# Kernel optimization log

Measured on AMD Instinct MI355X. Metric: run time of the kernel, lower is better.

The kernel has to match this reference:

```python
import jax, jax.numpy as jnp
import numpy as np

B, N, D = 8, 512, 768
HS = 64          # gp_head_size
NT = 12          # len(tag_vocab)
NEG = 1e12


def setup_inputs() -> dict:
    key = jax.random.key(0)
    ks = jax.random.split(key, 14)
    s = 0.02  # init scale for weights
    return {
        "chars": jax.random.normal(ks[0], (B, N, D), dtype=jnp.float32),
        "mask": jax.random.randint(ks[1], (B, N), 0, 2).astype(jnp.int32),
        "w1_ent": jax.random.normal(ks[2], (2 * HS, D), dtype=jnp.float32) * s,
        "b1_ent": jax.random.normal(ks[3], (2 * HS,), dtype=jnp.float32) * s,
        "w2_ent": jax.random.normal(ks[4], (2 * 2, 2 * HS), dtype=jnp.float32) * s,
        "b2_ent": jax.random.normal(ks[5], (2 * 2,), dtype=jnp.float32) * s,
        "w1_head": jax.random.normal(ks[6], (2 * HS, D), dtype=jnp.float32) * s,
        "b1_head": jax.random.normal(ks[7], (2 * HS,), dtype=jnp.float32) * s,
        "w2_head": jax.random.normal(ks[8], (2 * NT, 2 * HS), dtype=jnp.float32) * s,
        "b2_head": jax.random.normal(ks[9], (2 * NT,), dtype=jnp.float32) * s,
        "w1_tail": jax.random.normal(ks[10], (2 * HS, D), dtype=jnp.float32) * s,
        "b1_tail": jax.random.normal(ks[11], (2 * HS,), dtype=jnp.float32) * s,
        "w2_tail": jax.random.normal(ks[12], (2 * NT, 2 * HS), dtype=jnp.float32) * s,
        "b2_tail": jax.random.normal(ks[13], (2 * NT,), dtype=jnp.float32) * s,
    }


def _egp(x, w1, b1, w2, b2, mask, head_size, rope, tril):
    # x: [B,N,D] -> h: [B,N,2*head_size]
    h = jnp.einsum('bnd,ed->bne', x, w1) + b1
    qw, kw = h[..., 0::2], h[..., 1::2]          # [B,N,head_size] each
    if rope:
        n = x.shape[1]
        pos = jnp.arange(n, dtype=x.dtype)
        inv = jnp.power(10000.0, -2.0 * jnp.arange(head_size // 2, dtype=x.dtype) / head_size)
        ang = pos[:, None] * inv[None, :]         # [N, head_size/2]
        cos = jnp.repeat(jnp.cos(ang), 2, axis=-1)[None]  # [1,N,head_size]
        sin = jnp.repeat(jnp.sin(ang), 2, axis=-1)[None]
        def rot(t):
            t2 = jnp.stack([-t[..., 1::2], t[..., 0::2]], axis=-1).reshape(t.shape)
            return t * cos + t2 * sin
        qw, kw = rot(qw), rot(kw)
    logits = jnp.einsum('bmd,bnd->bmn', qw, kw) / (head_size ** 0.5)  # [B,M,N]
    bias = (jnp.einsum('bne,he->bnh', h, w2) + b2).transpose(0, 2, 1) / 2.0  # [B,2H,N]
    # [B,H,M,N]
    logits = logits[:, None] + bias[:, 0::2, None, :] + bias[:, 1::2, :, None]
    m = mask.astype(logits.dtype)
    pad = 1.0 - m[:, None, None, :] * m[:, None, :, None]
    logits = logits - pad * NEG
    if tril:
        tri = jnp.tril(jnp.ones((logits.shape[-2], logits.shape[-1]), logits.dtype), k=-1)
        logits = logits - tri * NEG
    return logits


def reference(chars, mask, w1_ent, b1_ent, w2_ent, b2_ent,
              w1_head, b1_head, w2_head, b2_head,
              w1_tail, b1_tail, w2_tail, b2_tail):
    entity = _egp(chars, w1_ent, b1_ent, w2_ent, b2_ent, mask, HS, True, True)
    head = _egp(chars, w1_head, b1_head, w2_head, b2_head, mask, HS, False, False)
    tail = _egp(chars, w1_tail, b1_tail, w2_tail, b2_tail, mask, HS, False, False)
    return (entity, head, tail)
```

## Files before the change

kernel.cpp:

```cpp
#include <hip/hip_runtime.h>
#include <cstddef>

namespace {
constexpr int B_ = 8;
constexpr int N_ = 512;
constexpr int D_ = 768;
constexpr int HS_ = 64;
constexpr int M_ = B_ * N_;
constexpr int E_ = 2 * HS_;
constexpr float NEGV = 1000000000000.0f;
constexpr float LOG2_10000 = 13.287712379549449f;
}

typedef short mfrag_t __attribute__((ext_vector_type(8)));
typedef short mhalf_t __attribute__((ext_vector_type(4)));
typedef float macc_t  __attribute__((ext_vector_type(4)));
typedef float vf4_t   __attribute__((ext_vector_type(4)));

__device__ __forceinline__ unsigned short bft(float x) {
    union { float f; unsigned u; } c; c.f = x;
    return (unsigned short)(c.u >> 16);
}
__device__ __forceinline__ unsigned short bfrne(float x) {
    union { float f; unsigned u; } c; c.f = x;
    const unsigned r = c.u + 0x7FFFu + ((c.u >> 16) & 1u);
    return (unsigned short)(r >> 16);
}

__global__ __launch_bounds__(256) void prep_kernel(
    const float* __restrict__ chars,
    const float* __restrict__ w1e, const float* __restrict__ b1e,
    const float* __restrict__ w2e, const float* __restrict__ b2e,
    const float* __restrict__ w1h, const float* __restrict__ b1h,
    const float* __restrict__ w2h, const float* __restrict__ b2h,
    const float* __restrict__ w1t, const float* __restrict__ b1t,
    const float* __restrict__ w2t, const float* __restrict__ b2t,
    unsigned short* __restrict__ qbf, unsigned short* __restrict__ kbf,
    float* __restrict__ bias_e, float* __restrict__ bias_h, float* __restrict__ bias_t)
{
    const int fam = blockIdx.y;
    const float* w1 = (fam == 0) ? w1e : (fam == 1) ? w1h : w1t;
    const float* b1 = (fam == 0) ? b1e : (fam == 1) ? b1h : b1t;
    const float* w2 = (fam == 0) ? w2e : (fam == 1) ? w2h : w2t;
    const float* b2 = (fam == 0) ? b2e : (fam == 1) ? b2h : b2t;
    float* bout = (fam == 0) ? bias_e : (fam == 1) ? bias_h : bias_t;
    const int H2 = (fam == 0) ? 4 : 24;
    unsigned short* qout = qbf + (size_t)fam * M_ * HS_;
    unsigned short* kout = kbf + (size_t)fam * M_ * HS_;
    const int m0 = blockIdx.x * 32;

    __shared__ unsigned short A_lds[32][40];
    __shared__ unsigned short B_lds[128][40];
    __shared__ float hs[32][132];

    const int t    = threadIdx.x;
    const int w    = t >> 6;
    const int lane = t & 63;
    const int ml   = lane & 15;
    const int quad = lane >> 4;
    const int wr16 = (w & 1) * 16;
    const int wc64 = (w >> 1) * 64;

    const int ar = t >> 3;
    const int ak = (t & 7) * 4;
    const int bc = t >> 1;
    const int bk = (t & 1) * 16;

    const float* aptr = chars + (size_t)(m0 + ar) * D_ + ak;
    const float* bptr = w1 + (size_t)bc * D_ + bk;

    macc_t acc[4];
    #pragma unroll
    for (int f = 0; f < 4; ++f) acc[f] = (macc_t)0.0f;

    float4 av0 = *(const float4*)(aptr);
    float4 bv0 = *(const float4*)(bptr);
    float4 bv1 = *(const float4*)(bptr + 4);
    float4 bv2 = *(const float4*)(bptr + 8);
    float4 bv3 = *(const float4*)(bptr + 12);

    for (int s = 0; s < 24; ++s) {
        {
            mhalf_t pa;
            pa[0] = (short)bft(av0.x); pa[1] = (short)bft(av0.y);
            pa[2] = (short)bft(av0.z); pa[3] = (short)bft(av0.w);
            *(mhalf_t*)&A_lds[ar][ak] = pa;
            mfrag_t pb0, pb1;
            pb0[0] = (short)bft(bv0.x); pb0[1] = (short)bft(bv0.y);
            pb0[2] = (short)bft(bv0.z); pb0[3] = (short)bft(bv0.w);
            pb0[4] = (short)bft(bv1.x); pb0[5] = (short)bft(bv1.y);
            pb0[6] = (short)bft(bv1.z); pb0[7] = (short)bft(bv1.w);
            pb1[0] = (short)bft(bv2.x); pb1[1] = (short)bft(bv2.y);
            pb1[2] = (short)bft(bv2.z); pb1[3] = (short)bft(bv2.w);
            pb1[4] = (short)bft(bv3.x); pb1[5] = (short)bft(bv3.y);
            pb1[6] = (short)bft(bv3.z); pb1[7] = (short)bft(bv3.w);
            *(mfrag_t*)&B_lds[bc][bk]     = pb0;
            *(mfrag_t*)&B_lds[bc][bk + 8] = pb1;
        }
        __syncthreads();
        if (s < 23) {
            aptr += 32; bptr += 32;
            av0 = *(const float4*)(aptr);
            bv0 = *(const float4*)(bptr);
            bv1 = *(const float4*)(bptr + 4);
            bv2 = *(const float4*)(bptr + 8);
            bv3 = *(const float4*)(bptr + 12);
        }
        const mfrag_t afrag = *(const mfrag_t*)&A_lds[wr16 + ml][quad * 8];
        #pragma unroll
        for (int f = 0; f < 4; ++f) {
            const mfrag_t bfrag = *(const mfrag_t*)&B_lds[wc64 + f * 16 + ml][quad * 8];
            acc[f] = __builtin_amdgcn_mfma_f32_16x16x32_bf16(afrag, bfrag, acc[f], 0, 0, 0);
        }
        __syncthreads();
    }

    #pragma unroll
    for (int f = 0; f < 4; ++f) {
        const int col = wc64 + f * 16 + ml;
        const float bb1 = b1[col];
        #pragma unroll
        for (int r = 0; r < 4; ++r)
            hs[wr16 + quad * 4 + r][col] = acc[f][r] + bb1;
    }
    __syncthreads();

    {
        const int row = t >> 3;
        const int kg  = t & 7;
        const float pos = (float)((m0 & 511) + row);
        unsigned short qv[8], kv[8];
        #pragma unroll
        for (int p = 0; p < 4; ++p) {
            const int i = kg * 4 + p;
            const float q0 = hs[row][4 * i + 0];
            const float k0 = hs[row][4 * i + 1];
            const float q1 = hs[row][4 * i + 2];
            const float k1 = hs[row][4 * i + 3];
            if (fam == 0) {
                const float inv = exp2f(-(float)i * (LOG2_10000 / 32.0f));
                float sn, cs;
                sincosf(pos * inv, &sn, &cs);
                qv[2 * p + 0] = bfrne(q0 * cs - q1 * sn);
                qv[2 * p + 1] = bfrne(q1 * cs + q0 * sn);
                kv[2 * p + 0] = bfrne(k0 * cs - k1 * sn);
                kv[2 * p + 1] = bfrne(k1 * cs + k0 * sn);
            } else {
                qv[2 * p + 0] = bfrne(q0);
                qv[2 * p + 1] = bfrne(q1);
                kv[2 * p + 0] = bfrne(k0);
                kv[2 * p + 1] = bfrne(k1);
            }
        }
        unsigned short* qp = qout + (size_t)(m0 + row) * HS_ + kg * 8;
        unsigned short* kp = kout + (size_t)(m0 + row) * HS_ + kg * 8;
        *(mfrag_t*)qp = *(const mfrag_t*)&qv[0];
        *(mfrag_t*)kp = *(const mfrag_t*)&kv[0];
    }

    {
        const int row = t & 31;
        const int h2b = t >> 5;
        const int bb  = m0 >> 9;
        const int nb  = (m0 & 511) + row;
        float accv[3] = {0, 0, 0};
        for (int e0 = 0; e0 < E_; e0 += 16) {
            float4 hv0 = *(const float4*)&hs[row][e0];
            float4 hv1 = *(const float4*)&hs[row][e0 + 4];
            float4 hv2 = *(const float4*)&hs[row][e0 + 8];
            float4 hv3 = *(const float4*)&hs[row][e0 + 12];
            int p = 0;
            for (int h2 = h2b; h2 < H2; h2 += 8, ++p) {
                const float* wr = w2 + (size_t)h2 * E_ + e0;
                const float4 w0 = *(const float4*)(wr);
                const float4 w1v = *(const float4*)(wr + 4);
                const float4 w2v = *(const float4*)(wr + 8);
                const float4 w3v = *(const float4*)(wr + 12);
                accv[p] += hv0.x * w0.x + hv0.y * w0.y + hv0.z * w0.z + hv0.w * w0.w
                         + hv1.x * w1v.x + hv1.y * w1v.y + hv1.z * w1v.z + hv1.w * w1v.w
                         + hv2.x * w2v.x + hv2.y * w2v.y + hv2.z * w2v.z + hv2.w * w2v.w
                         + hv3.x * w3v.x + hv3.y * w3v.y + hv3.z * w3v.z + hv3.w * w3v.w;
            }
        }
        int p = 0;
        for (int h2 = h2b; h2 < H2; h2 += 8, ++p)
            bout[((size_t)bb * H2 + h2) * N_ + nb] = (accv[p] + b2[h2]) * 0.5f;
    }
}

template <int H, bool TRIL>
__device__ __forceinline__ void egp_tile(
    const unsigned short* __restrict__ qf, const unsigned short* __restrict__ kf,
    const float* __restrict__ biasfam, const int* __restrict__ mask,
    float* __restrict__ out, int b, int m0, int n0, float (*Cs)[68], int t)
{
    const int w    = t >> 6;
    const int lane = t & 63;
    const int ml   = lane & 15;
    const int quad = lane >> 4;

    macc_t acc[4];
    #pragma unroll
    for (int f = 0; f < 4; ++f) acc[f] = (macc_t)0.0f;

    const unsigned short* qrow = qf + (size_t)(b * N_ + m0 + w * 16 + ml) * HS_ + quad * 8;
    const unsigned short* krow = kf + (size_t)(b * N_ + n0 + ml) * HS_ + quad * 8;

    #pragma unroll
    for (int s = 0; s < 2; ++s) {
        const mfrag_t af = *(const mfrag_t*)(qrow + s * 32);
        #pragma unroll
        for (int f = 0; f < 4; ++f) {
            const mfrag_t bf = *(const mfrag_t*)(krow + (size_t)f * 16 * HS_ + s * 32);
            acc[f] = __builtin_amdgcn_mfma_f32_16x16x32_bf16(af, bf, acc[f], 0, 0, 0);
        }
    }

    #pragma unroll
    for (int f = 0; f < 4; ++f)
        #pragma unroll
        for (int r = 0; r < 4; ++r)
            Cs[w * 16 + quad * 4 + r][f * 16 + ml] = acc[f][r] * 0.125f;
    __syncthreads();

    const int rq = t >> 4;
    const int cq = t & 15;

    float4 av[4];
    #pragma unroll
    for (int j = 0; j < 4; ++j) av[j] = *(const float4*)&Cs[4 * rq + j][4 * cq];

    int mrow[4], mm[4];
    #pragma unroll
    for (int j = 0; j < 4; ++j) {
        mrow[j] = m0 + 4 * rq + j;
        mm[j]   = mask[b * N_ + mrow[j]];
    }
    const int ncol = n0 + 4 * cq;
    const int4 mnv = *(const int4*)(mask + b * N_ + ncol);
    const int mn[4] = { mnv.x, mnv.y, mnv.z, mnv.w };

    #pragma unroll
    for (int hh = 0; hh < H; ++hh) {
        const float4 be = *(const float4*)(biasfam + ((size_t)b * 2 * H + 2 * hh) * N_ + ncol);
        float bo[4];
        #pragma unroll
        for (int j = 0; j < 4; ++j)
            bo[j] = biasfam[((size_t)b * 2 * H + 2 * hh + 1) * N_ + mrow[j]];

        #pragma unroll
        for (int j = 0; j < 4; ++j) {
            const float* aj = (const float*)&av[j];
            float o[4] = { aj[0] + be.x + bo[j], aj[1] + be.y + bo[j],
                           aj[2] + be.z + bo[j], aj[3] + be.w + bo[j] };
            #pragma unroll
            for (int q = 0; q < 4; ++q) {
                if (!(mm[j] & mn[q])) o[q] -= NEGV;
                if (TRIL && (ncol + q) < mrow[j]) o[q] -= NEGV;
            }
            vf4_t ov;
            ov.x = o[0]; ov.y = o[1]; ov.z = o[2]; ov.w = o[3];
            __builtin_nontemporal_store(
                ov, (vf4_t*)(out + ((size_t)(b * H + hh) * N_ + mrow[j]) * N_ + ncol));
        }
    }
}

__global__ __launch_bounds__(256) void egp_all_kernel(
    const unsigned short* __restrict__ qbf, const unsigned short* __restrict__ kbf,
    const float* __restrict__ bias_e, const float* __restrict__ bias_h,
    const float* __restrict__ bias_t,
    const int* __restrict__ mask, float* __restrict__ out)
{
    __shared__ float Cs[64][68];

    const int t   = threadIdx.x;
    const int m0  = blockIdx.x * 64;
    const int n0  = blockIdx.y * 64;
    const int fam = blockIdx.z >> 3;
    const int b   = blockIdx.z & 7;

    const size_t ent_sz  = (size_t)B_ * 2 * N_ * N_;
    const size_t head_sz = (size_t)B_ * 12 * N_ * N_;
    const size_t fsl = (size_t)M_ * HS_;

    if (fam == 0) {
        egp_tile<2, true>(qbf, kbf, bias_e, mask, out, b, m0, n0, Cs, t);
    } else if (fam == 1) {
        egp_tile<12, false>(qbf + fsl, kbf + fsl, bias_h, mask,
                            out + ent_sz, b, m0, n0, Cs, t);
    } else {
        egp_tile<12, false>(qbf + 2 * fsl, kbf + 2 * fsl, bias_t, mask,
                            out + ent_sz + head_sz, b, m0, n0, Cs, t);
    }
}

extern "C" void kernel_launch(void* const* d_in, const int* in_sizes, int n_in,
                              void* d_out, int out_size, void* d_ws, size_t ws_size,
                              hipStream_t stream)
{
    const float* chars = (const float*)d_in[0];
    const int*   mask  = (const int*)d_in[1];
    const float* w1e = (const float*)d_in[2];
    const float* b1e = (const float*)d_in[3];
    const float* w2e = (const float*)d_in[4];
    const float* b2e = (const float*)d_in[5];
    const float* w1h = (const float*)d_in[6];
    const float* b1h = (const float*)d_in[7];
    const float* w2h = (const float*)d_in[8];
    const float* b2h = (const float*)d_in[9];
    const float* w1t = (const float*)d_in[10];
    const float* b1t = (const float*)d_in[11];
    const float* w2t = (const float*)d_in[12];
    const float* b2t = (const float*)d_in[13];

    float* out = (float*)d_out;

    unsigned short* qbf = (unsigned short*)d_ws;
    unsigned short* kbf = qbf + (size_t)3 * M_ * HS_;
    float* bias_e = (float*)(kbf + (size_t)3 * M_ * HS_);
    float* bias_h = bias_e + (size_t)B_ * 4 * N_;
    float* bias_t = bias_h + (size_t)B_ * 24 * N_;

    prep_kernel<<<dim3(128, 3), 256, 0, stream>>>(
        chars, w1e, b1e, w2e, b2e, w1h, b1h, w2h, b2h, w1t, b1t, w2t, b2t,
        qbf, kbf, bias_e, bias_h, bias_t);

    egp_all_kernel<<<dim3(8, 8, 24), 256, 0, stream>>>(
        qbf, kbf, bias_e, bias_h, bias_t, mask, out);
}
```

Baseline: 283.1 us.

## Split prep kernel output columns in half to double block count

The prep kernel now splits the 128-wide projection output into two 64-column halves handled by separate blocks, doubling the grid from 384 to 768 blocks. Each half writes a partial bias sum to its own buffer, and the main kernel adds the two partial bias buffers when reading them. This is meant to improve occupancy and parallelism of the small projection GEMM on the many-CU GPU. In exchange, the chars tile is loaded and converted twice, and the main kernel does extra bias loads and adds.

```diff
diff --git a/kernel.cpp b/kernel.cpp
--- a/kernel.cpp
+++ b/kernel.cpp
@@ -38,20 +38,23 @@
     unsigned short* __restrict__ qbf, unsigned short* __restrict__ kbf,
     float* __restrict__ bias_e, float* __restrict__ bias_h, float* __restrict__ bias_t)
 {
-    const int fam = blockIdx.y;
+    const int fam  = blockIdx.y >> 1;
+    const int half = blockIdx.y & 1;
     const float* w1 = (fam == 0) ? w1e : (fam == 1) ? w1h : w1t;
     const float* b1 = (fam == 0) ? b1e : (fam == 1) ? b1h : b1t;
     const float* w2 = (fam == 0) ? w2e : (fam == 1) ? w2h : w2t;
     const float* b2 = (fam == 0) ? b2e : (fam == 1) ? b2h : b2t;
-    float* bout = (fam == 0) ? bias_e : (fam == 1) ? bias_h : bias_t;
     const int H2 = (fam == 0) ? 4 : 24;
+    float* bout = ((fam == 0) ? bias_e : (fam == 1) ? bias_h : bias_t)
+                  + (size_t)half * B_ * H2 * N_;
     unsigned short* qout = qbf + (size_t)fam * M_ * HS_;
     unsigned short* kout = kbf + (size_t)fam * M_ * HS_;
     const int m0 = blockIdx.x * 32;
+    const int c0 = half * 64;
 
     __shared__ unsigned short A_lds[32][40];
-    __shared__ unsigned short B_lds[128][40];
-    __shared__ float hs[32][132];
+    __shared__ unsigned short B_lds[64][40];
+    __shared__ float hs[32][68];
 
     const int t    = threadIdx.x;
     const int w    = t >> 6;
@@ -59,25 +62,22 @@
     const int ml   = lane & 15;
     const int quad = lane >> 4;
     const int wr16 = (w & 1) * 16;
-    const int wc64 = (w >> 1) * 64;
+    const int wc32 = (w >> 1) * 32;
 
     const int ar = t >> 3;
     const int ak = (t & 7) * 4;
-    const int bc = t >> 1;
-    const int bk = (t & 1) * 16;
+    const int bc = t >> 2;
+    const int bk = (t & 3) * 8;
 
     const float* aptr = chars + (size_t)(m0 + ar) * D_ + ak;
-    const float* bptr = w1 + (size_t)bc * D_ + bk;
-
-    macc_t acc[4];
-    #pragma unroll
-    for (int f = 0; f < 4; ++f) acc[f] = (macc_t)0.0f;
+    const float* bptr = w1 + (size_t)(c0 + bc) * D_ + bk;
+
+    macc_t acc[2];
+    acc[0] = (macc_t)0.0f; acc[1] = (macc_t)0.0f;
 
     float4 av0 = *(const float4*)(aptr);
     float4 bv0 = *(const float4*)(bptr);
     float4 bv1 = *(const float4*)(bptr + 4);
-    float4 bv2 = *(const float4*)(bptr + 8);
-    float4 bv3 = *(const float4*)(bptr + 12);
 
     for (int s = 0; s < 24; ++s) {
         {
@@ -85,17 +85,12 @@
             pa[0] = (short)bft(av0.x); pa[1] = (short)bft(av0.y);
             pa[2] = (short)bft(av0.z); pa[3] = (short)bft(av0.w);
             *(mhalf_t*)&A_lds[ar][ak] = pa;
-            mfrag_t pb0, pb1;
-            pb0[0] = (short)bft(bv0.x); pb0[1] = (short)bft(bv0.y);
-            pb0[2] = (short)bft(bv0.z); pb0[3] = (short)bft(bv0.w);
-            pb0[4] = (short)bft(bv1.x); pb0[5] = (short)bft(bv1.y);
-            pb0[6] = (short)bft(bv1.z); pb0[7] = (short)bft(bv1.w);
-            pb1[0] = (short)bft(bv2.x); pb1[1] = (short)bft(bv2.y);
-            pb1[2] = (short)bft(bv2.z); pb1[3] = (short)bft(bv2.w);
-            pb1[4] = (short)bft(bv3.x); pb1[5] = (short)bft(bv3.y);
-            pb1[6] = (short)bft(bv3.z); pb1[7] = (short)bft(bv3.w);
-            *(mfrag_t*)&B_lds[bc][bk]     = pb0;
-            *(mfrag_t*)&B_lds[bc][bk + 8] = pb1;
+            mfrag_t pb;
+            pb[0] = (short)bft(bv0.x); pb[1] = (short)bft(bv0.y);
+            pb[2] = (short)bft(bv0.z); pb[3] = (short)bft(bv0.w);
+            pb[4] = (short)bft(bv1.x); pb[5] = (short)bft(bv1.y);
+            pb[6] = (short)bft(bv1.z); pb[7] = (short)bft(bv1.w);
+            *(mfrag_t*)&B_lds[bc][bk] = pb;
         }
         __syncthreads();
         if (s < 23) {
@@ -103,22 +98,20 @@
             av0 = *(const float4*)(aptr);
             bv0 = *(const float4*)(bptr);
             bv1 = *(const float4*)(bptr + 4);
-            bv2 = *(const float4*)(bptr + 8);
-            bv3 = *(const float4*)(bptr + 12);
         }
         const mfrag_t afrag = *(const mfrag_t*)&A_lds[wr16 + ml][quad * 8];
         #pragma unroll
-        for (int f = 0; f < 4; ++f) {
-            const mfrag_t bfrag = *(const mfrag_t*)&B_lds[wc64 + f * 16 + ml][quad * 8];
+        for (int f = 0; f < 2; ++f) {
+            const mfrag_t bfrag = *(const mfrag_t*)&B_lds[wc32 + f * 16 + ml][quad * 8];
             acc[f] = __builtin_amdgcn_mfma_f32_16x16x32_bf16(afrag, bfrag, acc[f], 0, 0, 0);
         }
         __syncthreads();
     }
 
     #pragma unroll
-    for (int f = 0; f < 4; ++f) {
-        const int col = wc64 + f * 16 + ml;
-        const float bb1 = b1[col];
+    for (int f = 0; f < 2; ++f) {
+        const int col = wc32 + f * 16 + ml;
+        const float bb1 = b1[c0 + col];
         #pragma unroll
         for (int r = 0; r < 4; ++r)
             hs[wr16 + quad * 4 + r][col] = acc[f][r] + bb1;
@@ -129,16 +122,17 @@
         const int row = t >> 3;
         const int kg  = t & 7;
         const float pos = (float)((m0 & 511) + row);
-        unsigned short qv[8], kv[8];
-        #pragma unroll
-        for (int p = 0; p < 4; ++p) {
-            const int i = kg * 4 + p;
-            const float q0 = hs[row][4 * i + 0];
-            const float k0 = hs[row][4 * i + 1];
-            const float q1 = hs[row][4 * i + 2];
-            const float k1 = hs[row][4 * i + 3];
+        unsigned short qv[4], kv[4];
+        #pragma unroll
+        for (int p = 0; p < 2; ++p) {
+            const int il = kg * 2 + p;
+            const float q0 = hs[row][4 * il + 0];
+            const float k0 = hs[row][4 * il + 1];
+            const float q1 = hs[row][4 * il + 2];
+            const float k1 = hs[row][4 * il + 3];
             if (fam == 0) {
-                const float inv = exp2f(-(float)i * (LOG2_10000 / 32.0f));
+                const int ig = half * 16 + il;
+                const float inv = exp2f(-(float)ig * (LOG2_10000 / 32.0f));
                 float sn, cs;
                 sincosf(pos * inv, &sn, &cs);
                 qv[2 * p + 0] = bfrne(q0 * cs - q1 * sn);
@@ -152,10 +146,9 @@
                 kv[2 * p + 1] = bfrne(k1);
             }
         }
-        unsigned short* qp = qout + (size_t)(m0 + row) * HS_ + kg * 8;
-        unsigned short* kp = kout + (size_t)(m0 + row) * HS_ + kg * 8;
-        *(mfrag_t*)qp = *(const mfrag_t*)&qv[0];
-        *(mfrag_t*)kp = *(const mfrag_t*)&kv[0];
+        const size_t off = (size_t)(m0 + row) * HS_ + half * 32 + kg * 4;
+        *(mhalf_t*)(qout + off) = *(const mhalf_t*)&qv[0];
+        *(mhalf_t*)(kout + off) = *(const mhalf_t*)&kv[0];
     }
 
     {
@@ -164,14 +157,14 @@
         const int bb  = m0 >> 9;
         const int nb  = (m0 & 511) + row;
         float accv[3] = {0, 0, 0};
-        for (int e0 = 0; e0 < E_; e0 += 16) {
+        for (int e0 = 0; e0 < 64; e0 += 16) {
             float4 hv0 = *(const float4*)&hs[row][e0];
             float4 hv1 = *(const float4*)&hs[row][e0 + 4];
             float4 hv2 = *(const float4*)&hs[row][e0 + 8];
             float4 hv3 = *(const float4*)&hs[row][e0 + 12];
             int p = 0;
             for (int h2 = h2b; h2 < H2; h2 += 8, ++p) {
-                const float* wr = w2 + (size_t)h2 * E_ + e0;
+                const float* wr = w2 + (size_t)h2 * E_ + c0 + e0;
                 const float4 w0 = *(const float4*)(wr);
                 const float4 w1v = *(const float4*)(wr + 4);
                 const float4 w2v = *(const float4*)(wr + 8);
@@ -183,15 +176,18 @@
             }
         }
         int p = 0;
-        for (int h2 = h2b; h2 < H2; h2 += 8, ++p)
-            bout[((size_t)bb * H2 + h2) * N_ + nb] = (accv[p] + b2[h2]) * 0.5f;
+        for (int h2 = h2b; h2 < H2; h2 += 8, ++p) {
+            const float bterm = (half == 0) ? b2[h2] : 0.0f;
+            bout[((size_t)bb * H2 + h2) * N_ + nb] = (accv[p] + bterm) * 0.5f;
+        }
     }
 }
 
 template <int H, bool TRIL>
 __device__ __forceinline__ void egp_tile(
     const unsigned short* __restrict__ qf, const unsigned short* __restrict__ kf,
-    const float* __restrict__ biasfam, const int* __restrict__ mask,
+    const float* __restrict__ bias0, const float* __restrict__ bias1,
+    const int* __restrict__ mask,
     float* __restrict__ out, int b, int m0, int n0, float (*Cs)[68], int t)
 {
     const int w    = t >> 6;
@@ -242,11 +238,17 @@
 
     #pragma unroll
     for (int hh = 0; hh < H; ++hh) {
-        const float4 be = *(const float4*)(biasfam + ((size_t)b * 2 * H + 2 * hh) * N_ + ncol);
+        const size_t be_idx = ((size_t)b * 2 * H + 2 * hh) * N_ + ncol;
+        const float4 be0 = *(const float4*)(bias0 + be_idx);
+        const float4 be1 = *(const float4*)(bias1 + be_idx);
+        const float4 be = make_float4(be0.x + be1.x, be0.y + be1.y,
+                                      be0.z + be1.z, be0.w + be1.w);
         float bo[4];
         #pragma unroll
-        for (int j = 0; j < 4; ++j)
-            bo[j] = biasfam[((size_t)b * 2 * H + 2 * hh + 1) * N_ + mrow[j]];
+        for (int j = 0; j < 4; ++j) {
+            const size_t bo_idx = ((size_t)b * 2 * H + 2 * hh + 1) * N_ + mrow[j];
+            bo[j] = bias0[bo_idx] + bias1[bo_idx];
+        }
 
         #pragma unroll
         for (int j = 0; j < 4; ++j) {
@@ -283,14 +285,16 @@
     const size_t ent_sz  = (size_t)B_ * 2 * N_ * N_;
     const size_t head_sz = (size_t)B_ * 12 * N_ * N_;
     const size_t fsl = (size_t)M_ * HS_;
+    const size_t ehalf = (size_t)B_ * 4 * N_;
+    const size_t hhalf = (size_t)B_ * 24 * N_;
 
     if (fam == 0) {
-        egp_tile<2, true>(qbf, kbf, bias_e, mask, out, b, m0, n0, Cs, t);
+        egp_tile<2, true>(qbf, kbf, bias_e, bias_e + ehalf, mask, out, b, m0, n0, Cs, t);
     } else if (fam == 1) {
-        egp_tile<12, false>(qbf + fsl, kbf + fsl, bias_h, mask,
+        egp_tile<12, false>(qbf + fsl, kbf + fsl, bias_h, bias_h + hhalf, mask,
                             out + ent_sz, b, m0, n0, Cs, t);
     } else {
-        egp_tile<12, false>(qbf + 2 * fsl, kbf + 2 * fsl, bias_t, mask,
+        egp_tile<12, false>(qbf + 2 * fsl, kbf + 2 * fsl, bias_t, bias_t + hhalf, mask,
                             out + ent_sz + head_sz, b, m0, n0, Cs, t);
     }
 }
@@ -319,10 +323,10 @@
     unsigned short* qbf = (unsigned short*)d_ws;
     unsigned short* kbf = qbf + (size_t)3 * M_ * HS_;
     float* bias_e = (float*)(kbf + (size_t)3 * M_ * HS_);
-    float* bias_h = bias_e + (size_t)B_ * 4 * N_;
-    float* bias_t = bias_h + (size_t)B_ * 24 * N_;
-
-    prep_kernel<<<dim3(128, 3), 256, 0, stream>>>(
+    float* bias_h = bias_e + (size_t)2 * B_ * 4 * N_;
+    float* bias_t = bias_h + (size_t)2 * B_ * 24 * N_;
+
+    prep_kernel<<<dim3(128, 6), 256, 0, stream>>>(
         chars, w1e, b1e, w2e, b2e, w1h, b1h, w2h, b2h, w1t, b1t, w2t, b2t,
         qbf, kbf, bias_e, bias_h, bias_t);
 
```

Measured after the change: 276.5 us. 2.3% less time.
